# Optimization experiments

Measured on AMD Instinct MI355X. Metric: run time of the kernel, lower is better.

Reference implementation:

```python
import jax, jax.numpy as jnp
import numpy as np
from jax import lax

D_STATE, D_ADAPT, D_CNN, D_RNN, D_OUT, HORIZON = 12, 16, 64, 256, 2, 10
B, L, H, W = 32, 16, 112, 112
DN = ('NCHW', 'OIHW', 'NCHW')
BN_EPS = 1e-5


def setup_inputs() -> dict:
    key = jax.random.key(0)
    ks = jax.random.split(key, 22)
    rn = lambda k, shape, s=0.05: jax.random.normal(k, shape, jnp.float32) * s
    return {
        'x': jax.random.normal(ks[0], (B, L, D_STATE), jnp.float32),
        'frames': jax.random.normal(ks[1], (B, L, 3, H, W), jnp.float32),
        # backbone `cnn`: 16x16 stride-16 patchify conv 3 -> 576 (gives 7x7 spatial)
        'cnn_w': rn(ks[2], (576, 3, 16, 16)), 'cnn_b': rn(ks[3], (576,)),
        # cnn_1: Conv2d(576, 64, 3, padding=1) + ReLU + BatchNorm (eval) + Dropout (eval=identity)
        'cnn1_w': rn(ks[4], (D_CNN, 576, 3, 3)), 'cnn1_b': rn(ks[5], (D_CNN,)),
        'bn_g': jnp.ones((D_CNN,), jnp.float32), 'bn_b': jnp.zeros((D_CNN,), jnp.float32),
        'bn_m': jnp.zeros((D_CNN,), jnp.float32), 'bn_v': jnp.ones((D_CNN,), jnp.float32),
        'a0_w': rn(ks[6], (D_ADAPT, D_STATE)), 'a0_b': rn(ks[7], (D_ADAPT,)),
        'ai_w': rn(ks[8], (D_ADAPT, D_ADAPT)), 'ai_b': rn(ks[9], (D_ADAPT,)),
        'an_w': rn(ks[10], (D_RNN, D_CNN + D_ADAPT)), 'an_b': rn(ks[11], (D_RNN,)),
        # single-layer batch_first GRU, PyTorch gate layout [r, z, n]
        'w_ih': rn(ks[12], (3 * D_RNN, D_RNN)), 'w_hh': rn(ks[13], (3 * D_RNN, D_RNN)),
        'b_ih': rn(ks[14], (3 * D_RNN,)), 'b_hh': rn(ks[15], (3 * D_RNN,)),
        'fi_w': rn(ks[16], (D_RNN, D_RNN)), 'fi_b': rn(ks[17], (D_RNN,)),
        'fn_w': rn(ks[18], (D_OUT, D_RNN)), 'fn_b': rn(ks[19], (D_OUT,)),
    }


def _gru_cell(xt, h, w_ih, w_hh, b_ih, b_hh):
    gi = xt @ w_ih.T + b_ih  # (B, 3*D)
    gh = h @ w_hh.T + b_hh
    i_r, i_z, i_n = jnp.split(gi, 3, axis=-1)
    h_r, h_z, h_n = jnp.split(gh, 3, axis=-1)
    r = jax.nn.sigmoid(i_r + h_r)
    z = jax.nn.sigmoid(i_z + h_z)
    n = jnp.tanh(i_n + r * h_n)
    return (1.0 - z) * n + z * h


def _forward(x, frames, cnn_w, cnn_b, cnn1_w, cnn1_b, bn_g, bn_b, bn_m, bn_v,
             a0_w, a0_b, ai_w, ai_b, an_w, an_b, w_ih, w_hh, b_ih, b_hh,
             fi_w, fi_b, fn_w, fn_b):
    b, l = frames.shape[0], frames.shape[1]
    f = frames.reshape((-1,) + frames.shape[-3:])  # (b*l, 3, H, W)
    # backbone cnn: patchify conv -> (b*l, 576, 7, 7)
    f = lax.conv_general_dilated(f, cnn_w, (16, 16), 'VALID', dimension_numbers=DN) + cnn_b[:, None, None]
    # cnn_1: Conv3x3 same -> ReLU -> BatchNorm(eval) -> Dropout(eval=identity)
    f = lax.conv_general_dilated(f, cnn1_w, (1, 1), 'SAME', dimension_numbers=DN) + cnn1_b[:, None, None]
    f = jax.nn.relu(f)
    inv = bn_g / jnp.sqrt(bn_v + BN_EPS)
    f = (f - bn_m[:, None, None]) * inv[:, None, None] + bn_b[:, None, None]
    # AdaptiveAvgPool2d((1,1)) then reshape to (b, l, d_cnn)
    f = f.mean(axis=(2, 3)).reshape(b, l, -1)
    # state adapters
    s = jax.nn.relu(x @ a0_w.T + a0_b)
    s = s + jax.nn.relu(s @ ai_w.T + ai_b)
    s = jnp.concatenate([s, f], axis=-1)  # (b, l, d_cnn + d_adapt)
    s = jax.nn.relu(s @ an_w.T + an_b)    # (b, l, d_rnn)
    # encoder GRU over the l frames
    d_rnn = w_hh.shape[1]
    h0 = jnp.zeros((b, d_rnn), s.dtype)
    def enc_step(h, xt):
        h2 = _gru_cell(xt, h, w_ih, w_hh, b_ih, b_hh)
        return h2, None
    h, _ = lax.scan(enc_step, h0, jnp.swapaxes(s, 0, 1))
    x_in = h  # last output of single-layer GRU == final hidden state
    def dec_step(carry, _):
        xi, hh = carry
        hn = _gru_cell(xi, hh, w_ih, w_hh, b_ih, b_hh)  # one GRU step; output == new hidden
        xr = hn + jax.nn.relu(hn @ fi_w.T + fi_b)       # final_i residual
        pred = jnp.tanh(xr @ fn_w.T + fn_b)             # final_n head
        return (xr, hn), pred
    _, preds = lax.scan(dec_step, (x_in, h), None, length=HORIZON)
    return preds[:, :, None, :]  # (horizon, b, 1, d_out) matching torch.stack of (b,1,d_out)


def reference(x, frames, cnn_w, cnn_b, cnn1_w, cnn1_b, bn_g, bn_b, bn_m, bn_v,
              a0_w, a0_b, ai_w, ai_b, an_w, an_b, w_ih, w_hh, b_ih, b_hh,
              fi_w, fi_b, fn_w, fn_b):
    return _forward(x, frames, cnn_w, cnn_b, cnn1_w, cnn1_b, bn_g, bn_b, bn_m, bn_v,
                    a0_w, a0_b, ai_w, ai_b, an_w, an_b, w_ih, w_hh, b_ih, b_hh,
                    fi_w, fi_b, fn_w, fn_b)
```

## Files before the change

kernel.cpp:

```cpp
#include <hip/hip_runtime.h>

typedef unsigned short u16;
typedef unsigned int u32;
typedef __bf16 bf16x8 __attribute__((ext_vector_type(8)));
typedef float f32x4 __attribute__((ext_vector_type(4)));
typedef unsigned short u16x8 __attribute__((ext_vector_type(8)));
typedef unsigned int u32x4 __attribute__((ext_vector_type(4)));
typedef _Float16 v2h __attribute__((ext_vector_type(2)));

__device__ __forceinline__ u16 f2bf(float f) {
    unsigned u = __float_as_uint(f);
    u = (u + 0x7fffu + ((u >> 16) & 1u)) >> 16;
    return (u16)u;
}
__device__ __forceinline__ float bf2f(u16 h) {
    return __uint_as_float((unsigned)h << 16);
}
__device__ __forceinline__ u32 packh2(float a, float b) {
    _Float16 ha = (_Float16)a, hb = (_Float16)b;
    u16 la = __builtin_bit_cast(u16, ha), lb = __builtin_bit_cast(u16, hb);
    return (u32)la | ((u32)lb << 16);
}
__device__ __forceinline__ float dot2acc(u32 w, u32 h, float acc) {
#if __has_builtin(__builtin_amdgcn_fdot2)
    return __builtin_amdgcn_fdot2(__builtin_bit_cast(v2h, w),
                                  __builtin_bit_cast(v2h, h), acc, false);
#else
    v2h wv = __builtin_bit_cast(v2h, w), hv = __builtin_bit_cast(v2h, h);
    return acc + (float)wv.x * (float)hv.x + (float)wv.y * (float)hv.y;
#endif
}
__device__ __forceinline__ float dot8(u32x4 w, u32x4 h, float acc) {
    acc = dot2acc(w.x, h.x, acc);
    acc = dot2acc(w.y, h.y, acc);
    acc = dot2acc(w.z, h.z, acc);
    acc = dot2acc(w.w, h.w, acc);
    return acc;
}
__device__ __forceinline__ void gload_lds16(const void* g, void* l) {
    __builtin_amdgcn_global_load_lds(
        (const __attribute__((address_space(1))) unsigned int*)g,
        (__attribute__((address_space(3))) unsigned int*)l, 16, 0, 0);
}

__global__ __launch_bounds__(256) void prep_kernel(
    const float* __restrict__ cnn_w, const float* __restrict__ cnn1_w,
    const float* __restrict__ w_hh, const float* __restrict__ w_ih,
    const float* __restrict__ fi_w, const float* __restrict__ frames,
    u16* __restrict__ B1, u16* __restrict__ B2,
    u32* __restrict__ whh8, u32* __restrict__ wih8, u32* __restrict__ fi8,
    u32* __restrict__ zpage, u16* __restrict__ fbf)
{
    if (blockIdx.x >= 3924) {
        size_t i = ((size_t)(blockIdx.x - 3924) * 256 + threadIdx.x) * 8;
        float4 a = *(const float4*)(frames + i);
        float4 b = *(const float4*)(frames + i + 4);
        u16x8 v = { f2bf(a.x), f2bf(a.y), f2bf(a.z), f2bf(a.w),
                    f2bf(b.x), f2bf(b.y), f2bf(b.z), f2bf(b.w) };
        __builtin_nontemporal_store(v, (u16x8*)(fbf + i));
        return;
    }
    int idx = blockIdx.x * 256 + threadIdx.x;
    if (idx < 442368) { B1[idx] = f2bf(cnn_w[idx]); return; }
    idx -= 442368;
    if (idx < 331776) {
        int n = idx / 5184, rem = idx - n * 5184;
        int off = rem / 576, c = rem - off * 576;
        int dy = off / 3, dx = off - dy * 3;
        B2[idx] = f2bf(cnn1_w[((n * 576 + c) * 3 + dy) * 3 + dx]);
        return;
    }
    idx -= 331776;
    if (idx < 98304) {
        int kb = idx / 3072, r = idx - kb * 3072;
        int o = r >> 2, c = r & 3;
        int kk = kb * 8 + c * 2;
        whh8[idx] = packh2(w_hh[o * 256 + kk], w_hh[o * 256 + kk + 1]);
        return;
    }
    idx -= 98304;
    if (idx < 98304) {
        int kb = idx / 3072, r = idx - kb * 3072;
        int o = r >> 2, c = r & 3;
        int kk = kb * 8 + c * 2;
        wih8[idx] = packh2(w_ih[o * 256 + kk], w_ih[o * 256 + kk + 1]);
        return;
    }
    idx -= 98304;
    if (idx < 32768) {
        int kb = idx / 1024, r = idx - kb * 1024;
        int u = r >> 2, c = r & 3;
        int kk = kb * 8 + c * 2;
        fi8[idx] = packh2(fi_w[u * 256 + kk], fi_w[u * 256 + kk + 1]);
        return;
    }
    idx -= 32768;
    if (idx < 1024) zpage[idx] = 0u;
}

__global__ __launch_bounds__(256) void gemm1_v2(
    const u16* __restrict__ fbf, const u16* __restrict__ B1,
    const float* __restrict__ cnn_b, u16* __restrict__ f1)
{
    __shared__ u16 As[128 * 64];
    __shared__ u16 Bs[64 * 64];
    const int t = threadIdx.x, bx = blockIdx.x;
    const int m0 = (bx / 9) * 128, n0 = (bx % 9) * 64;
    const int wave = t >> 6, lane = t & 63;
    const int lm = lane & 15, lq = lane >> 4;

    f32x4 acc[2][4];
#pragma unroll
    for (int i = 0; i < 2; ++i)
#pragma unroll
        for (int q = 0; q < 4; ++q) acc[i][q] = (f32x4){0.f, 0.f, 0.f, 0.f};

    int ac8[4]; size_t abase[4];
#pragma unroll
    for (int i = 0; i < 4; ++i) {
        int s = wave * 256 + i * 64 + lane;
        int row = s >> 3, cc = s & 7;
        ac8[i] = cc ^ (row & 7);
        int m = m0 + row;
        int fr = m / 49, pos = m - fr * 49;
        int py = pos / 7, px = pos - py * 7;
        abase[i] = (size_t)fr * 37632 + py * 1792 + px * 16;
    }
    int bn[2], bc8[2];
#pragma unroll
    for (int i = 0; i < 2; ++i) {
        int s = wave * 128 + i * 64 + lane;
        int n = s >> 3, cc = s & 7;
        bn[i] = n; bc8[i] = cc ^ (n & 7);
    }

    for (int kt = 0; kt < 12; ++kt) {
        const int k0 = kt * 64;
#pragma unroll
        for (int i = 0; i < 4; ++i) {
            int k = k0 + ac8[i] * 8;
            int c = k >> 8, dy = (k >> 4) & 15, dx = k & 15;
            gload_lds16(fbf + abase[i] + c * 12544 + dy * 112 + dx,
                        &As[(wave * 256 + i * 64) * 8]);
        }
#pragma unroll
        for (int i = 0; i < 2; ++i) {
            gload_lds16(B1 + (size_t)(n0 + bn[i]) * 768 + k0 + bc8[i] * 8,
                        &Bs[(wave * 128 + i * 64) * 8]);
        }
        __syncthreads();
#pragma unroll
        for (int s = 0; s < 2; ++s) {
            bf16x8 a[2], b[4];
#pragma unroll
            for (int mi = 0; mi < 2; ++mi) {
                int row = wave * 32 + mi * 16 + lm;
                int c8 = s * 4 + lq;
                a[mi] = *(const bf16x8*)(&As[(row * 8 + (c8 ^ (row & 7))) * 8]);
            }
#pragma unroll
            for (int q = 0; q < 4; ++q) {
                int n = q * 16 + lm;
                int c8 = s * 4 + lq;
                b[q] = *(const bf16x8*)(&Bs[(n * 8 + (c8 ^ (n & 7))) * 8]);
            }
#pragma unroll
            for (int mi = 0; mi < 2; ++mi)
#pragma unroll
                for (int q = 0; q < 4; ++q)
                    acc[mi][q] = __builtin_amdgcn_mfma_f32_16x16x32_bf16(a[mi], b[q], acc[mi][q], 0, 0, 0);
        }
        __syncthreads();
    }
#pragma unroll
    for (int mi = 0; mi < 2; ++mi) {
#pragma unroll
        for (int q = 0; q < 4; ++q) {
            int n = n0 + q * 16 + lm;
            float bias = cnn_b[n];
#pragma unroll
            for (int r = 0; r < 4; ++r) {
                int m = m0 + wave * 32 + mi * 16 + lq * 4 + r;
                __builtin_nontemporal_store(f2bf(acc[mi][q][r] + bias), &f1[(size_t)m * 576 + n]);
            }
        }
    }
}

__global__ __launch_bounds__(256) void gemm1_patchify(
    const float* __restrict__ frames, const u16* __restrict__ B1,
    const float* __restrict__ cnn_b, u16* __restrict__ f1)
{
    __shared__ u16 As[128 * 64];
    __shared__ u16 Bs[64 * 64];
    const int t = threadIdx.x;
    const int bx = blockIdx.x;
    const int m0 = (bx / 9) * 128;
    const int n0 = (bx % 9) * 64;
    const int wave = t >> 6, lane = t & 63;
    const int lm = lane & 15, lq = lane >> 4;

    f32x4 acc[2][4];
#pragma unroll
    for (int i = 0; i < 2; ++i)
#pragma unroll
        for (int q = 0; q < 4; ++q) acc[i][q] = (f32x4){0.f, 0.f, 0.f, 0.f};

    int arow[4], ac8[4], abase[4];
#pragma unroll
    for (int i = 0; i < 4; ++i) {
        int cid = t + i * 256;
        int row = cid >> 3, c8 = cid & 7;
        int m = m0 + row;
        int fr = m / 49, pos = m - fr * 49;
        int py = pos / 7, px = pos - py * 7;
        arow[i] = row; ac8[i] = c8;
        abase[i] = (fr * 3 * 112 + py * 16) * 112 + px * 16;
    }

    for (int kt = 0; kt < 12; ++kt) {
        const int k0 = kt * 64;
#pragma unroll
        for (int i = 0; i < 4; ++i) {
            int k = k0 + ac8[i] * 8;
            int c = k >> 8, dy = (k >> 4) & 15, dx = k & 15;
            const float* src = frames + abase[i] + (c * 112 + dy) * 112 + dx;
            float4 v0 = *(const float4*)src;
            float4 v1 = *(const float4*)(src + 4);
            u16x8 v = { f2bf(v0.x), f2bf(v0.y), f2bf(v0.z), f2bf(v0.w),
                        f2bf(v1.x), f2bf(v1.y), f2bf(v1.z), f2bf(v1.w) };
            int sidx = arow[i] * 8 + (ac8[i] ^ (arow[i] & 7));
            *(u16x8*)(&As[sidx * 8]) = v;
        }
#pragma unroll
        for (int i = 0; i < 2; ++i) {
            int cid = t + i * 256;
            int n = cid >> 3, c8 = cid & 7;
            u16x8 v = *(const u16x8*)(B1 + (size_t)(n0 + n) * 768 + k0 + c8 * 8);
            int sidx = n * 8 + (c8 ^ (n & 7));
            *(u16x8*)(&Bs[sidx * 8]) = v;
        }
        __syncthreads();
#pragma unroll
        for (int s = 0; s < 2; ++s) {
            bf16x8 a[2], b[4];
#pragma unroll
            for (int mi = 0; mi < 2; ++mi) {
                int row = wave * 32 + mi * 16 + lm;
                int c8 = s * 4 + lq;
                a[mi] = *(const bf16x8*)(&As[(row * 8 + (c8 ^ (row & 7))) * 8]);
            }
#pragma unroll
            for (int q = 0; q < 4; ++q) {
                int n = q * 16 + lm;
                int c8 = s * 4 + lq;
                b[q] = *(const bf16x8*)(&Bs[(n * 8 + (c8 ^ (n & 7))) * 8]);
            }
#pragma unroll
            for (int mi = 0; mi < 2; ++mi)
#pragma unroll
                for (int q = 0; q < 4; ++q)
                    acc[mi][q] = __builtin_amdgcn_mfma_f32_16x16x32_bf16(a[mi], b[q], acc[mi][q], 0, 0, 0);
        }
        __syncthreads();
    }
#pragma unroll
    for (int mi = 0; mi < 2; ++mi) {
#pragma unroll
        for (int q = 0; q < 4; ++q) {
            int n = n0 + q * 16 + lm;
            float bias = cnn_b[n];
#pragma unroll
            for (int r = 0; r < 4; ++r) {
                int m = m0 + wave * 32 + mi * 16 + lq * 4 + r;
                __builtin_nontemporal_store(f2bf(acc[mi][q][r] + bias), &f1[(size_t)m * 576 + n]);
            }
        }
    }
}

__global__ __launch_bounds__(256) void gemm2_v2(
    const u16* __restrict__ f1, const u16* __restrict__ B2,
    const u16* __restrict__ zpage, float* __restrict__ C2)
{
    __shared__ u16 As[64 * 64];
    __shared__ u16 Bs[64 * 64];
    const int t = threadIdx.x;
    const int m0 = blockIdx.x * 64;
    const int wave = t >> 6, lane = t & 63;
    const int lm = lane & 15, lq = lane >> 4;

    f32x4 acc[4];
#pragma unroll
    for (int q = 0; q < 4; ++q) acc[q] = (f32x4){0.f, 0.f, 0.f, 0.f};

    int ac8[2], afr[2], apy[2], apx[2];
#pragma unroll
    for (int i = 0; i < 2; ++i) {
        int s = wave * 128 + i * 64 + lane;
        int row = s >> 3, cc = s & 7;
        ac8[i] = cc ^ (row & 7);
        int m = m0 + row;
        int fr = m / 49, pos = m - fr * 49;
        int py = pos / 7;
        afr[i] = fr; apy[i] = py; apx[i] = pos - py * 7;
    }
    int bn[2], bc8[2];
#pragma unroll
    for (int i = 0; i < 2; ++i) {
        int s = wave * 128 + i * 64 + lane;
        int n = s >> 3, cc = s & 7;
        bn[i] = n; bc8[i] = cc ^ (n & 7);
    }

    for (int kt = 0; kt < 81; ++kt) {
        int off = kt / 9, cb = kt - off * 9;
        int dy = off / 3, dx = off - dy * 3;
        int c0 = cb * 64;
#pragma unroll
        for (int i = 0; i < 2; ++i) {
            int yy = apy[i] + dy - 1, xx = apx[i] + dx - 1;
            const u16* g = ((unsigned)yy < 7u && (unsigned)xx < 7u)
                ? f1 + ((size_t)(afr[i] * 49 + yy * 7 + xx)) * 576 + c0 + ac8[i] * 8
                : zpage;
            gload_lds16(g, &As[(wave * 128 + i * 64) * 8]);
        }
#pragma unroll
        for (int i = 0; i < 2; ++i) {
            gload_lds16(B2 + (size_t)bn[i] * 5184 + kt * 64 + bc8[i] * 8,
                        &Bs[(wave * 128 + i * 64) * 8]);
        }
        __syncthreads();
#pragma unroll
        for (int s = 0; s < 2; ++s) {
            int row = wave * 16 + lm;
            int c8 = s * 4 + lq;
            bf16x8 a = *(const bf16x8*)(&As[(row * 8 + (c8 ^ (row & 7))) * 8]);
            bf16x8 b[4];
#pragma unroll
            for (int q = 0; q < 4; ++q) {
                int n = q * 16 + lm;
                b[q] = *(const bf16x8*)(&Bs[(n * 8 + (c8 ^ (n & 7))) * 8]);
            }
#pragma unroll
            for (int q = 0; q < 4; ++q)
                acc[q] = __builtin_amdgcn_mfma_f32_16x16x32_bf16(a, b[q], acc[q], 0, 0, 0);
        }
        __syncthreads();
    }
#pragma unroll
    for (int q = 0; q < 4; ++q)
#pragma unroll
        for (int r = 0; r < 4; ++r) {
            int m = m0 + wave * 16 + lq * 4 + r;
            int n = q * 16 + lm;
            __builtin_nontemporal_store(acc[q][r], &C2[(size_t)m * 64 + n]);
        }
}

__global__ __launch_bounds__(256) void reduce_kernel(
    const float* __restrict__ C2, const float* __restrict__ cnn1_b,
    const float* __restrict__ bn_g, const float* __restrict__ bn_b,
    const float* __restrict__ bn_m, const float* __restrict__ bn_v,
    float* __restrict__ fmean)
{
    int idx = blockIdx.x * 256 + threadIdx.x;
    int bl = idx >> 6, ch = idx & 63;
    float bias = cnn1_b[ch];
    const float* p = C2 + (size_t)bl * 49 * 64 + ch;
    float s = 0.f;
#pragma unroll
    for (int i = 0; i < 49; ++i) s += fmaxf(p[i * 64] + bias, 0.f);
    float mean = s * (1.f / 49.f);
    float inv = bn_g[ch] * rsqrtf(bn_v[ch] + 1e-5f);
    fmean[idx] = (mean - bn_m[ch]) * inv + bn_b[ch];
}

__global__ __launch_bounds__(256) void adapt_prep2_kernel(
    const float* __restrict__ x, const float* __restrict__ fmean,
    const float* __restrict__ a0_w, const float* __restrict__ a0_b,
    const float* __restrict__ ai_w, const float* __restrict__ ai_b,
    const float* __restrict__ an_w, const float* __restrict__ an_b,
    const float* __restrict__ w_ih,
    u16* __restrict__ zx_hi, u16* __restrict__ zx_lo,
    u16* __restrict__ wih_hi, u16* __restrict__ wih_lo)
{
    const int t = threadIdx.x;
    if (blockIdx.x >= 512) {
        int idx = (blockIdx.x - 512) * 256 + t;
        float v = w_ih[idx];
        u16 hi = f2bf(v);
        wih_hi[idx] = hi;
        wih_lo[idx] = f2bf(v - bf2f(hi));
        return;
    }
    const int bl = blockIdx.x;
    __shared__ float s0[16];
    __shared__ float sf[80];
    if (t < 16) {
        float a = a0_b[t];
        const float* xp = x + bl * 12;
#pragma unroll
        for (int i = 0; i < 12; ++i) a += xp[i] * a0_w[t * 12 + i];
        s0[t] = fmaxf(a, 0.f);
    }
    __syncthreads();
    if (t < 16) {
        float a = ai_b[t];
#pragma unroll
        for (int i = 0; i < 16; ++i) a += s0[i] * ai_w[t * 16 + i];
        sf[t] = s0[t] + fmaxf(a, 0.f);
    } else if (t < 80) {
        sf[t] = fmean[bl * 64 + (t - 16)];
    }
    __syncthreads();
    float a = an_b[t];
#pragma unroll 8
    for (int i = 0; i < 80; ++i) a += sf[i] * an_w[t * 80 + i];
    a = fmaxf(a, 0.f);
    u16 hi = f2bf(a);
    zx_hi[bl * 256 + t] = hi;
    zx_lo[bl * 256 + t] = f2bf(a - bf2f(hi));
}

__global__ __launch_bounds__(256) void gi_kernel(
    const u16* __restrict__ zx_hi, const u16* __restrict__ zx_lo,
    const u16* __restrict__ wih_hi, const u16* __restrict__ wih_lo,
    const float* __restrict__ b_ih, float* __restrict__ gi_pre)
{
    __shared__ u16 Ah[128 * 64], Al[128 * 64];
    __shared__ u16 Bh[64 * 64], Bl[64 * 64];
    const int t = threadIdx.x, bx = blockIdx.x;
    const int m0 = (bx / 12) * 128, n0 = (bx % 12) * 64;
    const int wave = t >> 6, lane = t & 63;
    const int lm = lane & 15, lq = lane >> 4;

    f32x4 acc[2][4];
#pragma unroll
    for (int i = 0; i < 2; ++i)
#pragma unroll
        for (int q = 0; q < 4; ++q) acc[i][q] = (f32x4){0.f, 0.f, 0.f, 0.f};

    for (int kt = 0; kt < 4; ++kt) {
        const int k0 = kt * 64;
#pragma unroll
        for (int i = 0; i < 4; ++i) {
            int cid = t + i * 256;
            int row = cid >> 3, c8 = cid & 7;
            size_t src = (size_t)(m0 + row) * 256 + k0 + c8 * 8;
            int sidx = (row * 8 + (c8 ^ (row & 7))) * 8;
            *(u16x8*)(&Ah[sidx]) = *(const u16x8*)(zx_hi + src);
            *(u16x8*)(&Al[sidx]) = *(const u16x8*)(zx_lo + src);
        }
#pragma unroll
        for (int i = 0; i < 2; ++i) {
            int cid = t + i * 256;
            int n = cid >> 3, c8 = cid & 7;
            size_t src = (size_t)(n0 + n) * 256 + k0 + c8 * 8;
            int sidx = (n * 8 + (c8 ^ (n & 7))) * 8;
            *(u16x8*)(&Bh[sidx]) = *(const u16x8*)(wih_hi + src);
            *(u16x8*)(&Bl[sidx]) = *(const u16x8*)(wih_lo + src);
        }
        __syncthreads();
#pragma unroll
        for (int s = 0; s < 2; ++s) {
            bf16x8 ah[2], al[2], bh[4], blv[4];
#pragma unroll
            for (int mi = 0; mi < 2; ++mi) {
                int row = wave * 32 + mi * 16 + lm;
                int c8 = s * 4 + lq;
                int sidx = (row * 8 + (c8 ^ (row & 7))) * 8;
                ah[mi] = *(const bf16x8*)(&Ah[sidx]);
                al[mi] = *(const bf16x8*)(&Al[sidx]);
            }
#pragma unroll
            for (int q = 0; q < 4; ++q) {
                int n = q * 16 + lm;
                int c8 = s * 4 + lq;
                int sidx = (n * 8 + (c8 ^ (n & 7))) * 8;
                bh[q] = *(const bf16x8*)(&Bh[sidx]);
                blv[q] = *(const bf16x8*)(&Bl[sidx]);
            }
#pragma unroll
            for (int mi = 0; mi < 2; ++mi)
#pragma unroll
                for (int q = 0; q < 4; ++q) {
                    acc[mi][q] = __builtin_amdgcn_mfma_f32_16x16x32_bf16(ah[mi], bh[q], acc[mi][q], 0, 0, 0);
                    acc[mi][q] = __builtin_amdgcn_mfma_f32_16x16x32_bf16(ah[mi], blv[q], acc[mi][q], 0, 0, 0);
                    acc[mi][q] = __builtin_amdgcn_mfma_f32_16x16x32_bf16(al[mi], bh[q], acc[mi][q], 0, 0, 0);
                }
        }
        __syncthreads();
    }
#pragma unroll
    for (int q = 0; q < 4; ++q) {
        int n = n0 + q * 16 + lm;
        float bias = b_ih[n];
#pragma unroll
        for (int mi = 0; mi < 2; ++mi)
#pragma unroll
            for (int r = 0; r < 4; ++r) {
                int m = m0 + wave * 32 + mi * 16 + lq * 4 + r;
                gi_pre[(size_t)m * 768 + n] = acc[mi][q][r] + bias;
            }
    }
}

__global__ __launch_bounds__(768) void rnn_stream4(
    const float* __restrict__ gi_pre,
    const u32x4* __restrict__ whh8, const u32x4* __restrict__ wih8,
    const u32x4* __restrict__ fi8,
    const float* __restrict__ b_ih, const float* __restrict__ b_hh,
    const float* __restrict__ fi_b,
    const float* __restrict__ fn_w, const float* __restrict__ fn_b,
    float* __restrict__ out)
{
    extern __shared__ __align__(16) u32 slab[];
    const int b = blockIdx.x, t = threadIdx.x;
    const int wave = t >> 6;
    __shared__ __align__(16) u32 h2[128];
    __shared__ __align__(16) u32 x2[128];
    __shared__ float sA[768];
    __shared__ float sB[256];
    __shared__ float parts[768];
    __shared__ float pp[8];

#pragma unroll
    for (int j = 0; j < 12; ++j)
        *(u32x4*)&slab[(j * 768 + t) * 4] = whh8[j * 768 + t];

    u32x4 whr[8], wir[8];
#pragma unroll
    for (int j = 0; j < 8; ++j) whr[j] = whh8[(size_t)(12 + j) * 768 + t];
#pragma unroll
    for (int j = 0; j < 8; ++j) wir[j] = wih8[(size_t)j * 768 + t];

    const float bhh = b_hh[t];
    const float bih = b_ih[t];
    float hprev = 0.f;
    if (t < 128) h2[t] = 0u;
    __syncthreads();

    for (int l = 0; l < 16; ++l) {
        float gi = gi_pre[(size_t)(b * 16 + l) * 768 + t];
        float a0 = 0.f, a1 = 0.f;
#pragma unroll 4
        for (int j = 0; j < 12; ++j) {
            int jj = j + wave; if (jj >= 12) jj -= 12;
            int kb = 20 + jj;
            u32x4 w = whh8[(size_t)kb * 768 + t];
            u32x4 hh = *(const u32x4*)&h2[kb * 4];
            if (j & 1) a1 = dot8(w, hh, a1); else a0 = dot8(w, hh, a0);
        }
#pragma unroll
        for (int j = 0; j < 8; ++j) {
            u32x4 hh = *(const u32x4*)&h2[(12 + j) * 4];
            if (j & 1) a1 = dot8(whr[j], hh, a1); else a0 = dot8(whr[j], hh, a0);
        }
#pragma unroll
        for (int j = 0; j < 12; ++j) {
            u32x4 ws = *(const u32x4*)&slab[(j * 768 + t) * 4];
            u32x4 hh = *(const u32x4*)&h2[j * 4];
            if (j & 1) a1 = dot8(ws, hh, a1); else a0 = dot8(ws, hh, a0);
        }
        float ah = a0 + a1;
        if (t < 512) sA[t] = gi + ah + bhh;
        else { sA[t] = gi; sB[t - 512] = ah + bhh; }
        __syncthreads();
        if (t < 256) {
            float r = 1.f / (1.f + expf(-sA[t]));
            float z = 1.f / (1.f + expf(-sA[256 + t]));
            float n = tanhf(sA[512 + t] + r * sB[t]);
            hprev = (1.f - z) * n + z * hprev;
            float partner = __shfl_xor(hprev, 1);
            if ((t & 1) == 0) h2[t >> 1] = packh2(hprev, partner);
        }
        __syncthreads();
    }

    float xprev = hprev;
    if (t < 128) x2[t] = h2[t];
    __syncthreads();

    for (int d = 0; d < 10; ++d) {
        float a0 = 0.f, a1 = 0.f, x0 = 0.f, x1 = 0.f;
#pragma unroll 4
        for (int j = 0; j < 12; ++j) {
            int jj = j + wave; if (jj >= 12) jj -= 12;
            int kb = 20 + jj;
            u32x4 w = whh8[(size_t)kb * 768 + t];
            u32x4 hh = *(const u32x4*)&h2[kb * 4];
            if (j & 1) a1 = dot8(w, hh, a1); else a0 = dot8(w, hh, a0);
        }
#pragma unroll 4
        for (int j = 0; j < 24; ++j) {
            int jj = j + wave * 2; if (jj >= 24) jj -= 24;
            int kb = 8 + jj;
            u32x4 w = wih8[(size_t)kb * 768 + t];
            u32x4 xx = *(const u32x4*)&x2[kb * 4];
            if (j & 1) x1 = dot8(w, xx, x1); else x0 = dot8(w, xx, x0);
        }
#pragma unroll
        for (int j = 0; j < 8; ++j) {
            u32x4 hh = *(const u32x4*)&h2[(12 + j) * 4];
            u32x4 xx = *(const u32x4*)&x2[j * 4];
            if (j & 1) { a1 = dot8(whr[j], hh, a1); x1 = dot8(wir[j], xx, x1); }
            else       { a0 = dot8(whr[j], hh, a0); x0 = dot8(wir[j], xx, x0); }
        }
#pragma unroll
        for (int j = 0; j < 12; ++j) {
            u32x4 ws = *(const u32x4*)&slab[(j * 768 + t) * 4];
            u32x4 hh = *(const u32x4*)&h2[j * 4];
            if (j & 1) a1 = dot8(ws, hh, a1); else a0 = dot8(ws, hh, a0);
        }
        float ah = a0 + a1, ax = x0 + x1;
        if (t < 512) sA[t] = ax + bih + ah + bhh;
        else { sA[t] = ax + bih; sB[t - 512] = ah + bhh; }
        __syncthreads();
        if (t < 256) {
            float r = 1.f / (1.f + expf(-sA[t]));
            float z = 1.f / (1.f + expf(-sA[256 + t]));
            float n = tanhf(sA[512 + t] + r * sB[t]);
            hprev = (1.f - z) * n + z * hprev;
            float partner = __shfl_xor(hprev, 1);
            if ((t & 1) == 0) h2[t >> 1] = packh2(hprev, partner);
        }
        __syncthreads();
        {
            int u = t & 255, s = t >> 8;
            float afi = 0.f;
            for (int j = s; j < 32; j += 3) {
                u32x4 w = fi8[j * 256 + u];
                u32x4 hh = *(const u32x4*)&h2[j * 4];
                afi = dot8(w, hh, afi);
            }
            parts[t] = afi;
        }
        __syncthreads();
        if (t < 256) {
            float a = parts[t] + parts[256 + t] + parts[512 + t] + fi_b[t];
            xprev = hprev + fmaxf(a, 0.f);
            float partner = __shfl_xor(xprev, 1);
            if ((t & 1) == 0) x2[t >> 1] = packh2(xprev, partner);
            float c0 = xprev * fn_w[t];
            float c1 = xprev * fn_w[256 + t];
#pragma unroll
            for (int off = 32; off >= 1; off >>= 1) {
                c0 += __shfl_down(c0, off);
                c1 += __shfl_down(c1, off);
            }
            if ((t & 63) == 0) { pp[(t >> 6) * 2] = c0; pp[(t >> 6) * 2 + 1] = c1; }
        }
        __syncthreads();
        if (t < 2)
            out[d * 64 + b * 2 + t] =
                tanhf(fn_b[t] + pp[t] + pp[2 + t] + pp[4 + t] + pp[6 + t]);
    }
}

extern "C" void kernel_launch(void* const* d_in, const int* in_sizes, int n_in,
                              void* d_out, int out_size, void* d_ws, size_t ws_size,
                              hipStream_t stream)
{
    const float* x      = (const float*)d_in[0];
    const float* frames = (const float*)d_in[1];
    const float* cnn_w  = (const float*)d_in[2];
    const float* cnn_b  = (const float*)d_in[3];
    const float* cnn1_w = (const float*)d_in[4];
    const float* cnn1_b = (const float*)d_in[5];
    const float* bn_g   = (const float*)d_in[6];
    const float* bn_b   = (const float*)d_in[7];
    const float* bn_m   = (const float*)d_in[8];
    const float* bn_v   = (const float*)d_in[9];
    const float* a0_w   = (const float*)d_in[10];
    const float* a0_b   = (const float*)d_in[11];
    const float* ai_w   = (const float*)d_in[12];
    const float* ai_b   = (const float*)d_in[13];
    const float* an_w   = (const float*)d_in[14];
    const float* an_b   = (const float*)d_in[15];
    const float* w_ih   = (const float*)d_in[16];
    const float* w_hh   = (const float*)d_in[17];
    const float* b_ih   = (const float*)d_in[18];
    const float* b_hh   = (const float*)d_in[19];
    const float* fi_w   = (const float*)d_in[20];
    const float* fi_b   = (const float*)d_in[21];
    const float* fn_w   = (const float*)d_in[22];
    const float* fn_b   = (const float*)d_in[23];
    float* out = (float*)d_out;

    char* ws = (char*)d_ws;
    u16*   f1     = (u16*)(ws);
    u16*   B1     = (u16*)(ws + 28901376);
    u16*   B2     = (u16*)(ws + 29786112);
    float* C2     = (float*)(ws + 30449664);
    float* fmean  = (float*)(ws + 36872192);
    u32*   whh8   = (u32*)(ws + 37003264);
    u32*   wih8   = (u32*)(ws + 37396480);
    u32*   fi8    = (u32*)(ws + 37789696);
    u32*   zpage  = (u32*)(ws + 37920768);
    float* gi_pre = (float*)(ws + 30449664);
    u16*   wih_hi = (u16*)(ws + 32022528);
    u16*   wih_lo = (u16*)(ws + 32415744);
    u16*   zx_hi  = (u16*)(ws + 32808960);
    u16*   zx_lo  = (u16*)(ws + 33071104);
    u16*   fbf    = (u16*)(ws + 37924864);

    const bool big = ws_size >= 76460032ull;

    prep_kernel<<<big ? 13332 : 3924, 256, 0, stream>>>(
        cnn_w, cnn1_w, w_hh, w_ih, fi_w, frames,
        B1, B2, whh8, wih8, fi8, zpage, fbf);
    if (big) {
        gemm1_v2<<<196 * 9, 256, 0, stream>>>(fbf, B1, cnn_b, f1);
    } else {
        gemm1_patchify<<<196 * 9, 256, 0, stream>>>(frames, B1, cnn_b, f1);
    }
    gemm2_v2<<<392, 256, 0, stream>>>(f1, B2, (const u16*)zpage, C2);
    reduce_kernel<<<128, 256, 0, stream>>>(C2, cnn1_b, bn_g, bn_b, bn_m, bn_v, fmean);
    adapt_prep2_kernel<<<1280, 256, 0, stream>>>(x, fmean, a0_w, a0_b, ai_w, ai_b,
                                                 an_w, an_b, w_ih,
                                                 zx_hi, zx_lo, wih_hi, wih_lo);
    gi_kernel<<<48, 256, 0, stream>>>(zx_hi, zx_lo, wih_hi, wih_lo, b_ih, gi_pre);
    hipFuncSetAttribute((const void*)rnn_stream4,
                        hipFuncAttributeMaxDynamicSharedMemorySize, 147456);
    rnn_stream4<<<32, 768, 147456, stream>>>(gi_pre, (const u32x4*)whh8,
                                             (const u32x4*)wih8, (const u32x4*)fi8,
                                             b_ih, b_hh, fi_b, fn_w, fn_b, out);
}
```

Before: 421.0 us.

## Keep all non-slab W_hh blocks in registers, prefetch fi weights, lighter barriers

The RNN kernel now holds 20 of W_hh's k-blocks in registers instead of 8 plus 12 streamed from global memory each step. W_ih is now streamed fully from global in the decode loop rather than kept partly in registers. The fi weights are loaded into registers before the gate computation so their latency overlaps it. __syncthreads is replaced by an LDS-only waitcnt plus s_barrier. The larger register arrays raise pressure at 768 threads per block and may cause spills.

```diff
diff --git a/kernel.cpp b/kernel.cpp
--- a/kernel.cpp
+++ b/kernel.cpp
@@ -41,6 +41,10 @@
     __builtin_amdgcn_global_load_lds(
         (const __attribute__((address_space(1))) unsigned int*)g,
         (__attribute__((address_space(3))) unsigned int*)l, 16, 0, 0);
+}
+__device__ __forceinline__ void barrier_lds() {
+    __builtin_amdgcn_s_waitcnt(0xC07F);
+    __builtin_amdgcn_s_barrier();
 }
 
 __global__ __launch_bounds__(256) void prep_kernel(
@@ -506,7 +510,7 @@
     }
 }
 
-__global__ __launch_bounds__(768) void rnn_stream4(
+__global__ __launch_bounds__(768) void rnn_stream5(
     const float* __restrict__ gi_pre,
     const u32x4* __restrict__ whh8, const u32x4* __restrict__ wih8,
     const u32x4* __restrict__ fi8,
@@ -529,11 +533,9 @@
     for (int j = 0; j < 12; ++j)
         *(u32x4*)&slab[(j * 768 + t) * 4] = whh8[j * 768 + t];
 
-    u32x4 whr[8], wir[8];
-#pragma unroll
-    for (int j = 0; j < 8; ++j) whr[j] = whh8[(size_t)(12 + j) * 768 + t];
-#pragma unroll
-    for (int j = 0; j < 8; ++j) wir[j] = wih8[(size_t)j * 768 + t];
+    u32x4 whr[20];
+#pragma unroll
+    for (int j = 0; j < 20; ++j) whr[j] = whh8[(size_t)(12 + j) * 768 + t];
 
     const float bhh = b_hh[t];
     const float bih = b_ih[t];
@@ -544,29 +546,21 @@
     for (int l = 0; l < 16; ++l) {
         float gi = gi_pre[(size_t)(b * 16 + l) * 768 + t];
         float a0 = 0.f, a1 = 0.f;
-#pragma unroll 4
-        for (int j = 0; j < 12; ++j) {
-            int jj = j + wave; if (jj >= 12) jj -= 12;
-            int kb = 20 + jj;
-            u32x4 w = whh8[(size_t)kb * 768 + t];
-            u32x4 hh = *(const u32x4*)&h2[kb * 4];
-            if (j & 1) a1 = dot8(w, hh, a1); else a0 = dot8(w, hh, a0);
-        }
-#pragma unroll
-        for (int j = 0; j < 8; ++j) {
-            u32x4 hh = *(const u32x4*)&h2[(12 + j) * 4];
-            if (j & 1) a1 = dot8(whr[j], hh, a1); else a0 = dot8(whr[j], hh, a0);
-        }
 #pragma unroll
         for (int j = 0; j < 12; ++j) {
             u32x4 ws = *(const u32x4*)&slab[(j * 768 + t) * 4];
             u32x4 hh = *(const u32x4*)&h2[j * 4];
             if (j & 1) a1 = dot8(ws, hh, a1); else a0 = dot8(ws, hh, a0);
         }
+#pragma unroll
+        for (int j = 0; j < 20; ++j) {
+            u32x4 hh = *(const u32x4*)&h2[(12 + j) * 4];
+            if (j & 1) a1 = dot8(whr[j], hh, a1); else a0 = dot8(whr[j], hh, a0);
+        }
         float ah = a0 + a1;
         if (t < 512) sA[t] = gi + ah + bhh;
         else { sA[t] = gi; sB[t - 512] = ah + bhh; }
-        __syncthreads();
+        barrier_lds();
         if (t < 256) {
             float r = 1.f / (1.f + expf(-sA[t]));
             float z = 1.f / (1.f + expf(-sA[256 + t]));
@@ -575,37 +569,22 @@
             float partner = __shfl_xor(hprev, 1);
             if ((t & 1) == 0) h2[t >> 1] = packh2(hprev, partner);
         }
-        __syncthreads();
+        barrier_lds();
     }
 
     float xprev = hprev;
     if (t < 128) x2[t] = h2[t];
     __syncthreads();
+    const int u_ = t & 255, s_ = t >> 8;
 
     for (int d = 0; d < 10; ++d) {
         float a0 = 0.f, a1 = 0.f, x0 = 0.f, x1 = 0.f;
 #pragma unroll 4
-        for (int j = 0; j < 12; ++j) {
-            int jj = j + wave; if (jj >= 12) jj -= 12;
-            int kb = 20 + jj;
-            u32x4 w = whh8[(size_t)kb * 768 + t];
-            u32x4 hh = *(const u32x4*)&h2[kb * 4];
-            if (j & 1) a1 = dot8(w, hh, a1); else a0 = dot8(w, hh, a0);
-        }
-#pragma unroll 4
-        for (int j = 0; j < 24; ++j) {
-            int jj = j + wave * 2; if (jj >= 24) jj -= 24;
-            int kb = 8 + jj;
-            u32x4 w = wih8[(size_t)kb * 768 + t];
-            u32x4 xx = *(const u32x4*)&x2[kb * 4];
+        for (int j = 0; j < 32; ++j) {
+            int jj = (j + wave * 3) & 31;
+            u32x4 w = wih8[(size_t)jj * 768 + t];
+            u32x4 xx = *(const u32x4*)&x2[jj * 4];
             if (j & 1) x1 = dot8(w, xx, x1); else x0 = dot8(w, xx, x0);
-        }
-#pragma unroll
-        for (int j = 0; j < 8; ++j) {
-            u32x4 hh = *(const u32x4*)&h2[(12 + j) * 4];
-            u32x4 xx = *(const u32x4*)&x2[j * 4];
-            if (j & 1) { a1 = dot8(whr[j], hh, a1); x1 = dot8(wir[j], xx, x1); }
-            else       { a0 = dot8(whr[j], hh, a0); x0 = dot8(wir[j], xx, x0); }
         }
 #pragma unroll
         for (int j = 0; j < 12; ++j) {
@@ -613,10 +592,22 @@
             u32x4 hh = *(const u32x4*)&h2[j * 4];
             if (j & 1) a1 = dot8(ws, hh, a1); else a0 = dot8(ws, hh, a0);
         }
+#pragma unroll
+        for (int j = 0; j < 20; ++j) {
+            u32x4 hh = *(const u32x4*)&h2[(12 + j) * 4];
+            if (j & 1) a1 = dot8(whr[j], hh, a1); else a0 = dot8(whr[j], hh, a0);
+        }
         float ah = a0 + a1, ax = x0 + x1;
         if (t < 512) sA[t] = ax + bih + ah + bhh;
         else { sA[t] = ax + bih; sB[t - 512] = ah + bhh; }
-        __syncthreads();
+        barrier_lds();
+        u32x4 fw[11];
+        int cnt = 0;
+#pragma unroll
+        for (int j = 0; j < 11; ++j) {
+            int jj = s_ + j * 3;
+            if (jj < 32) { fw[j] = fi8[jj * 256 + u_]; cnt = j + 1; }
+        }
         if (t < 256) {
             float r = 1.f / (1.f + expf(-sA[t]));
             float z = 1.f / (1.f + expf(-sA[256 + t]));
@@ -625,18 +616,20 @@
             float partner = __shfl_xor(hprev, 1);
             if ((t & 1) == 0) h2[t >> 1] = packh2(hprev, partner);
         }
-        __syncthreads();
+        barrier_lds();
         {
-            int u = t & 255, s = t >> 8;
-            float afi = 0.f;
-            for (int j = s; j < 32; j += 3) {
-                u32x4 w = fi8[j * 256 + u];
-                u32x4 hh = *(const u32x4*)&h2[j * 4];
-                afi = dot8(w, hh, afi);
-            }
-            parts[t] = afi;
-        }
-        __syncthreads();
+            float f0 = 0.f, f1v = 0.f;
+#pragma unroll
+            for (int j = 0; j < 11; ++j) {
+                if (j < cnt) {
+                    int jj = s_ + j * 3;
+                    u32x4 hh = *(const u32x4*)&h2[jj * 4];
+                    if (j & 1) f1v = dot8(fw[j], hh, f1v); else f0 = dot8(fw[j], hh, f0);
+                }
+            }
+            parts[t] = f0 + f1v;
+        }
+        barrier_lds();
         if (t < 256) {
             float a = parts[t] + parts[256 + t] + parts[512 + t] + fi_b[t];
             xprev = hprev + fmaxf(a, 0.f);
@@ -651,7 +644,7 @@
             }
             if ((t & 63) == 0) { pp[(t >> 6) * 2] = c0; pp[(t >> 6) * 2 + 1] = c1; }
         }
-        __syncthreads();
+        barrier_lds();
         if (t < 2)
             out[d * 64 + b * 2 + t] =
                 tanhf(fn_b[t] + pp[t] + pp[2 + t] + pp[4 + t] + pp[6 + t]);
@@ -721,9 +714,9 @@
                                                  an_w, an_b, w_ih,
                                                  zx_hi, zx_lo, wih_hi, wih_lo);
     gi_kernel<<<48, 256, 0, stream>>>(zx_hi, zx_lo, wih_hi, wih_lo, b_ih, gi_pre);
-    hipFuncSetAttribute((const void*)rnn_stream4,
+    hipFuncSetAttribute((const void*)rnn_stream5,
                         hipFuncAttributeMaxDynamicSharedMemorySize, 147456);
-    rnn_stream4<<<32, 768, 147456, stream>>>(gi_pre, (const u32x4*)whh8,
+    rnn_stream5<<<32, 768, 147456, stream>>>(gi_pre, (const u32x4*)whh8,
                                              (const u32x4*)wih8, (const u32x4*)fi8,
                                              b_ih, b_hh, fi_b, fn_w, fn_b, out);
 }
```

After: 422.7 us. Within noise of the previous version (+0.4%).
